# Performance work log

Measured on AMD Instinct MI355X. Metric: run time of the kernel, lower is better.

## Reference

```python
import jax, jax.numpy as jnp
import numpy as np

IN_CH, OUT_CH = 256, 128
HID = 2 * OUT_CH  # 256
N_NODES, N_EDGES = 50000, 800000


def setup_inputs() -> dict:
    key = jax.random.key(0)
    k1, k2, k3, k4, k5, k6, k7 = jax.random.split(key, 7)
    feats = jax.random.normal(k1, (N_NODES, IN_CH), dtype=jnp.float32)
    src = jax.random.randint(k2, (N_EDGES,), 0, N_NODES, dtype=jnp.int64)
    dst = jax.random.randint(k3, (N_EDGES,), 0, N_NODES, dtype=jnp.int64)
    # GraphConv weights: layer0 in->2*out, layer1 2*out->out (Glorot-ish scale)
    W0 = jax.random.normal(k4, (IN_CH, HID), dtype=jnp.float32) / np.sqrt(IN_CH)
    b0 = jnp.zeros((HID,), dtype=jnp.float32)
    W1 = jax.random.normal(k5, (HID, OUT_CH), dtype=jnp.float32) / np.sqrt(HID)
    b1 = jnp.zeros((OUT_CH,), dtype=jnp.float32)
    return {"feats": feats, "src": src, "dst": dst, "W0": W0, "b0": b0, "W1": W1, "b1": b1}


def _graph_conv(x, W, b, src, dst, norm_src, norm_dst, n_nodes):
    # Apply W first (out <= in) to shrink the edge-gather intermediate, as DGL does.
    h = x @ W                                  # [N, out]
    h = h * norm_src[:, None]                  # D_src^-1/2
    msg = h[src]                               # [E, out] irregular gather
    agg = jax.ops.segment_sum(msg, dst, num_segments=n_nodes)  # SpMM
    agg = agg * norm_dst[:, None] + b          # D_dst^-1/2, bias
    return jax.nn.relu(agg)


def reference(feats, src, dst, W0, b0, W1, b1):
    n = feats.shape[0]
    loop = jnp.arange(n, dtype=src.dtype)
    src_sl = jnp.concatenate([src, loop])      # dgl.add_self_loop
    dst_sl = jnpp = jnp.concatenate([dst, loop])
    ones = jnp.ones_like(src_sl, dtype=feats.dtype)
    out_deg = jax.ops.segment_sum(ones, src_sl, num_segments=n)
    in_deg = jax.ops.segment_sum(ones, dst_sl, num_segments=n)
    norm_src = jax.lax.rsqrt(jnp.maximum(out_deg, 1.0))
    norm_dst = jax.lax.rsqrt(jnp.maximum(in_deg, 1.0))
    x = _graph_conv(feats, W0, b0, src_sl, dst_sl, norm_src, norm_dst, n)
    x = _graph_conv(x, W1, b1, src_sl, dst_sl, norm_src, norm_dst, n)
    return x
```

## Files before the change

kernel.cpp:

```cpp
#include <hip/hip_runtime.h>


typedef __attribute__((ext_vector_type(8))) short short8v;
typedef __attribute__((ext_vector_type(4))) float float4v;
typedef __attribute__((ext_vector_type(4))) _Float16 half4v;
typedef __attribute__((ext_vector_type(2))) _Float16 half2v;

__device__ inline unsigned short f2bf(float x) {
  unsigned u = __float_as_uint(x);
  return (unsigned short)((u + 0x7FFFu + ((u >> 16) & 1u)) >> 16);
}
__device__ inline float bf2f(unsigned short b) {
  return __uint_as_float(((unsigned)b) << 16);
}

__global__ __launch_bounds__(256) void k_hist8(const int* __restrict__ src,
                                               const int* __restrict__ dst,
                                               unsigned* __restrict__ cnt,
                                               int N, int E) {
  unsigned xcc;
  asm("s_getreg_b32 %0, hwreg(HW_REG_XCC_ID)" : "=s"(xcc));
  unsigned* my = cnt + (size_t)(xcc & 7) * 2u * (unsigned)N;
  int e = blockIdx.x * 256 + threadIdx.x;
  if (e < E) {
    __hip_atomic_fetch_add(&my[src[e]], 1u, __ATOMIC_RELAXED,
                           __HIP_MEMORY_SCOPE_WORKGROUP);
    __hip_atomic_fetch_add(&my[N + dst[e]], 1u, __ATOMIC_RELAXED,
                           __HIP_MEMORY_SCOPE_WORKGROUP);
  }
}

__global__ __launch_bounds__(256) void k_scan1_norm(
    const unsigned* __restrict__ cnt, int* __restrict__ part,
    int* __restrict__ bsums, float* __restrict__ nsrc,
    float* __restrict__ ndst, int N) {
  __shared__ int s[256];
  int t = threadIdx.x, g = blockIdx.x * 256 + t;
  int od = 0, id = 0;
  if (g < N) {
#pragma unroll
    for (int x = 0; x < 8; ++x) {
      od += cnt[(size_t)x * 2u * (unsigned)N + g];
      id += cnt[(size_t)x * 2u * (unsigned)N + N + g];
    }
    nsrc[g] = rsqrtf((float)(od + 1));
    ndst[g] = rsqrtf((float)(id + 1));
  }
  int v = (g < N) ? id : 0;
  s[t] = v;
  __syncthreads();
  for (int o = 1; o < 256; o <<= 1) {
    int add = (t >= o) ? s[t - o] : 0;
    __syncthreads();
    s[t] += add;
    __syncthreads();
  }
  if (g < N) part[g] = s[t] - v;
  if (t == 255) bsums[blockIdx.x] = s[255];
}

__global__ __launch_bounds__(256) void k_scan2(int* __restrict__ bsums, int nb) {
  __shared__ int s[256];
  int t = threadIdx.x;
  int v = (t < nb) ? bsums[t] : 0;
  s[t] = v;
  __syncthreads();
  for (int o = 1; o < 256; o <<= 1) {
    int add = (t >= o) ? s[t - o] : 0;
    __syncthreads();
    s[t] += add;
    __syncthreads();
  }
  if (t < nb) bsums[t] = s[t] - v;
}

__global__ __launch_bounds__(256) void k_scan3(int* __restrict__ part,
                                               int* __restrict__ cursor,
                                               const int* __restrict__ bsums,
                                               int N, int E) {
  int t = threadIdx.x, g = blockIdx.x * 256 + t;
  if (g < N) {
    int v = part[g] + bsums[blockIdx.x];
    part[g] = v;
    cursor[g] = v;
  }
  if (g == 0) part[N] = E;
}

__global__ __launch_bounds__(256) void k_fill(const int* __restrict__ src,
                                              const int* __restrict__ dst,
                                              int* __restrict__ cursor,
                                              int* __restrict__ colidx, int E) {
  int e = blockIdx.x * 256 + threadIdx.x;
  if (e < E) {
    int s = src[e];
    int p = atomicAdd(&cursor[dst[e]], 1);
    colidx[p] = s;
  }
}

__global__ __launch_bounds__(256) void k_wsplit(const float* __restrict__ W,
                                                short* __restrict__ WtH,
                                                short* __restrict__ WtL,
                                                int NCOL) {
  const int K = 256;
  int idx = blockIdx.x * 256 + threadIdx.x;
  if (idx >= K * NCOL) return;
  int k = idx & (K - 1);
  int n = idx >> 8;
  float v = W[(size_t)k * NCOL + n];
  unsigned short h = f2bf(v);
  unsigned short l = f2bf(v - bf2f(h));
  WtH[(size_t)n * K + k] = (short)h;
  WtL[(size_t)n * K + k] = (short)l;
}

template <int NCOL>
__global__ __launch_bounds__(256) void k_gemm_mfma(
    const float* __restrict__ A, const short* __restrict__ WtH,
    const short* __restrict__ WtL, const float* __restrict__ norm,
    _Float16* __restrict__ out, int M) {
  constexpr int K = 256, BM = 64, BK = 32, PAD = 40, NF = NCOL / 16;
  __shared__ short AH[BM][PAD], AL[BM][PAD];
  __shared__ short BH[NCOL][PAD], BL[NCOL][PAD];
  int tid = threadIdx.x;
  int w = tid >> 6, l = tid & 63;
  int lg = l >> 4, ln = l & 15;
  int row0 = blockIdx.x * BM;

  float4v acc[NF];
#pragma unroll
  for (int i = 0; i < NF; ++i) acc[i] = (float4v){0.f, 0.f, 0.f, 0.f};

  int ar = tid >> 2;
  int akq = (tid & 3) * 8;

  for (int k0 = 0; k0 < K; k0 += BK) {
    float av[8];
    int grow = row0 + ar;
    if (grow < M) {
      const float4* ap =
          reinterpret_cast<const float4*>(&A[(size_t)grow * K + k0 + akq]);
      float4 v0 = ap[0], v1 = ap[1];
      av[0] = v0.x; av[1] = v0.y; av[2] = v0.z; av[3] = v0.w;
      av[4] = v1.x; av[5] = v1.y; av[6] = v1.z; av[7] = v1.w;
    } else {
#pragma unroll
      for (int i = 0; i < 8; ++i) av[i] = 0.f;
    }
    short hh[8], ll[8];
#pragma unroll
    for (int i = 0; i < 8; ++i) {
      unsigned short h = f2bf(av[i]);
      hh[i] = (short)h;
      ll[i] = (short)f2bf(av[i] - bf2f(h));
    }
    *reinterpret_cast<short8v*>(&AH[ar][akq]) = *reinterpret_cast<short8v*>(hh);
    *reinterpret_cast<short8v*>(&AL[ar][akq]) = *reinterpret_cast<short8v*>(ll);

#pragma unroll
    for (int c = 0; c < NCOL / 64; ++c) {
      int chunk = c * 256 + tid;
      int bn = chunk >> 2, q = (chunk & 3) * 8;
      *reinterpret_cast<short8v*>(&BH[bn][q]) =
          *reinterpret_cast<const short8v*>(&WtH[(size_t)bn * K + k0 + q]);
      *reinterpret_cast<short8v*>(&BL[bn][q]) =
          *reinterpret_cast<const short8v*>(&WtL[(size_t)bn * K + k0 + q]);
    }
    __syncthreads();

    short8v aH = *reinterpret_cast<short8v*>(&AH[w * 16 + ln][lg * 8]);
    short8v aL = *reinterpret_cast<short8v*>(&AL[w * 16 + ln][lg * 8]);
#pragma unroll
    for (int nf = 0; nf < NF; ++nf) {
      short8v bHv = *reinterpret_cast<short8v*>(&BH[nf * 16 + ln][lg * 8]);
      short8v bLv = *reinterpret_cast<short8v*>(&BL[nf * 16 + ln][lg * 8]);
      acc[nf] = __builtin_amdgcn_mfma_f32_16x16x32_bf16(aH, bHv, acc[nf], 0, 0, 0);
      acc[nf] = __builtin_amdgcn_mfma_f32_16x16x32_bf16(aH, bLv, acc[nf], 0, 0, 0);
      acc[nf] = __builtin_amdgcn_mfma_f32_16x16x32_bf16(aL, bHv, acc[nf], 0, 0, 0);
    }
    __syncthreads();
  }

  int rbase = row0 + w * 16 + lg * 4;
  float nrm[4];
#pragma unroll
  for (int j = 0; j < 4; ++j)
    nrm[j] = (rbase + j < M) ? norm[rbase + j] : 0.f;
#pragma unroll
  for (int nf = 0; nf < NF; ++nf) {
#pragma unroll
    for (int j = 0; j < 4; ++j) {
      int r = rbase + j;
      if (r < M)
        out[(size_t)r * NCOL + nf * 16 + ln] = (_Float16)(acc[nf][j] * nrm[j]);
    }
  }
}

__global__ __launch_bounds__(256) void k_agg256(
    const _Float16* __restrict__ h, const int* __restrict__ rowptr,
    const int* __restrict__ colidx, const float* __restrict__ nd,
    const float* __restrict__ bias, float* __restrict__ out, int N) {
  int node = blockIdx.x * 4 + (threadIdx.x >> 6);
  int lane = threadIdx.x & 63;
  if (node >= N) return;
  const half4v* hv = reinterpret_cast<const half4v*>(h);
  half4v hs = hv[(size_t)node * 64 + lane];
  float4 acc;
  acc.x = (float)hs[0]; acc.y = (float)hs[1];
  acc.z = (float)hs[2]; acc.w = (float)hs[3];
  int e0 = rowptr[node], e1 = rowptr[node + 1];
  int e = e0;
  for (; e + 7 < e1; e += 8) {
    int si[8];
#pragma unroll
    for (int i = 0; i < 8; ++i) si[i] = colidx[e + i];
    half4v v[8];
#pragma unroll
    for (int i = 0; i < 8; ++i) v[i] = hv[(size_t)si[i] * 64 + lane];
#pragma unroll
    for (int i = 0; i < 8; ++i) {
      acc.x += (float)v[i][0]; acc.y += (float)v[i][1];
      acc.z += (float)v[i][2]; acc.w += (float)v[i][3];
    }
  }
  for (; e < e1; ++e) {
    half4v v0 = hv[(size_t)colidx[e] * 64 + lane];
    acc.x += (float)v0[0]; acc.y += (float)v0[1];
    acc.z += (float)v0[2]; acc.w += (float)v0[3];
  }
  float n = nd[node];
  float4 b = reinterpret_cast<const float4*>(bias)[lane];
  float4 r;
  r.x = fmaxf(fmaf(acc.x, n, b.x), 0.f);
  r.y = fmaxf(fmaf(acc.y, n, b.y), 0.f);
  r.z = fmaxf(fmaf(acc.z, n, b.z), 0.f);
  r.w = fmaxf(fmaf(acc.w, n, b.w), 0.f);
  reinterpret_cast<float4*>(out)[(size_t)node * 64 + lane] = r;
}

__global__ __launch_bounds__(256) void k_agg128(
    const _Float16* __restrict__ h, const int* __restrict__ rowptr,
    const int* __restrict__ colidx, const float* __restrict__ nd,
    const float* __restrict__ bias, float* __restrict__ out, int N) {
  int node = blockIdx.x * 4 + (threadIdx.x >> 6);
  int lane = threadIdx.x & 63;
  if (node >= N) return;
  const half2v* hv = reinterpret_cast<const half2v*>(h);
  half2v hs = hv[(size_t)node * 64 + lane];
  float2 acc;
  acc.x = (float)hs[0]; acc.y = (float)hs[1];
  int e0 = rowptr[node], e1 = rowptr[node + 1];
  int e = e0;
  for (; e + 7 < e1; e += 8) {
    int si[8];
#pragma unroll
    for (int i = 0; i < 8; ++i) si[i] = colidx[e + i];
    half2v v[8];
#pragma unroll
    for (int i = 0; i < 8; ++i) v[i] = hv[(size_t)si[i] * 64 + lane];
#pragma unroll
    for (int i = 0; i < 8; ++i) {
      acc.x += (float)v[i][0]; acc.y += (float)v[i][1];
    }
  }
  for (; e < e1; ++e) {
    half2v v0 = hv[(size_t)colidx[e] * 64 + lane];
    acc.x += (float)v0[0]; acc.y += (float)v0[1];
  }
  float n = nd[node];
  float2 b = reinterpret_cast<const float2*>(bias)[lane];
  float2 r;
  r.x = fmaxf(fmaf(acc.x, n, b.x), 0.f);
  r.y = fmaxf(fmaf(acc.y, n, b.y), 0.f);
  reinterpret_cast<float2*>(out)[(size_t)node * 64 + lane] = r;
}

extern "C" void kernel_launch(void* const* d_in, const int* in_sizes, int n_in,
                              void* d_out, int out_size, void* d_ws, size_t ws_size,
                              hipStream_t stream) {
  const float* feats = (const float*)d_in[0];
  const int* src = (const int*)d_in[1];
  const int* dst = (const int*)d_in[2];
  const float* W0 = (const float*)d_in[3];
  const float* b0 = (const float*)d_in[4];
  const float* W1 = (const float*)d_in[5];
  const float* b1 = (const float*)d_in[6];
  float* out = (float*)d_out;

  const int IN_CH = 256, HID = 256, OUT_CH = 128;
  int N = in_sizes[0] / IN_CH;
  int E = in_sizes[1];

  char* ws = (char*)d_ws;
  size_t off = 0;
  auto alloc = [&](size_t bytes) -> void* {
    void* p = ws + off;
    off += (bytes + 255) & ~(size_t)255;
    return p;
  };
  _Float16* h0 = (_Float16*)alloc((size_t)N * HID * 2);
  float* x1     = (float*)alloc((size_t)N * HID * 4);
  float* nsrc   = (float*)alloc((size_t)N * 4);
  float* ndst   = (float*)alloc((size_t)N * 4);
  unsigned* cnt = (unsigned*)alloc((size_t)8 * 2 * N * 4);
  int*   rowptr = (int*)alloc((size_t)(N + 1) * 4);
  int*   cursor = (int*)alloc((size_t)N * 4);
  int*   colidx = (int*)alloc((size_t)E * 4);
  int*   bsums  = (int*)alloc(1024);
  short* w0h    = (short*)alloc((size_t)HID * IN_CH * 2);
  short* w0l    = (short*)alloc((size_t)HID * IN_CH * 2);
  short* w1h    = (short*)alloc((size_t)OUT_CH * HID * 2);
  short* w1l    = (short*)alloc((size_t)OUT_CH * HID * 2);
  _Float16* h1  = h0;

  hipMemsetAsync(cnt, 0, (size_t)8 * 2 * N * 4, stream);

  int nbE = (E + 255) / 256, nbN = (N + 255) / 256;
  k_hist8<<<nbE, 256, 0, stream>>>(src, dst, cnt, N, E);
  k_scan1_norm<<<nbN, 256, 0, stream>>>(cnt, rowptr, bsums, nsrc, ndst, N);
  k_scan2<<<1, 256, 0, stream>>>(bsums, nbN);
  k_scan3<<<nbN, 256, 0, stream>>>(rowptr, cursor, bsums, N, E);
  k_fill<<<nbE, 256, 0, stream>>>(src, dst, cursor, colidx, E);

  k_wsplit<<<(IN_CH * HID) / 256, 256, 0, stream>>>(W0, w0h, w0l, HID);
  k_wsplit<<<(HID * OUT_CH) / 256, 256, 0, stream>>>(W1, w1h, w1l, OUT_CH);

  int gm = (N + 63) / 64;
  k_gemm_mfma<256><<<gm, 256, 0, stream>>>(feats, w0h, w0l, nsrc, h0, N);
  k_agg256<<<(N + 3) / 4, 256, 0, stream>>>(h0, rowptr, colidx, ndst, b0, x1, N);

  k_gemm_mfma<128><<<gm, 256, 0, stream>>>(x1, w1h, w1l, nsrc, h1, N);
  k_agg128<<<(N + 3) / 4, 256, 0, stream>>>(h1, rowptr, colidx, ndst, b1, out, N);
}
```

Baseline: 398.3 us.

## Slice aggregation by 32-channel column blocks and use per-XCC fill cursors

```diff
diff --git a/kernel.cpp b/kernel.cpp
--- a/kernel.cpp
+++ b/kernel.cpp
@@ -3,7 +3,6 @@
 
 typedef __attribute__((ext_vector_type(8))) short short8v;
 typedef __attribute__((ext_vector_type(4))) float float4v;
-typedef __attribute__((ext_vector_type(4))) _Float16 half4v;
 typedef __attribute__((ext_vector_type(2))) _Float16 half2v;
 
 __device__ inline unsigned short f2bf(float x) {
@@ -75,26 +74,37 @@
 }
 
 __global__ __launch_bounds__(256) void k_scan3(int* __restrict__ part,
-                                               int* __restrict__ cursor,
+                                               int* __restrict__ cursor8,
                                                const int* __restrict__ bsums,
+                                               const unsigned* __restrict__ cnt,
                                                int N, int E) {
   int t = threadIdx.x, g = blockIdx.x * 256 + t;
   if (g < N) {
     int v = part[g] + bsums[blockIdx.x];
     part[g] = v;
-    cursor[g] = v;
+    int run = v;
+#pragma unroll
+    for (int x = 0; x < 8; ++x) {
+      cursor8[(size_t)x * N + g] = run;
+      run += cnt[(size_t)x * 2u * (unsigned)N + N + g];
+    }
   }
   if (g == 0) part[N] = E;
 }
 
-__global__ __launch_bounds__(256) void k_fill(const int* __restrict__ src,
-                                              const int* __restrict__ dst,
-                                              int* __restrict__ cursor,
-                                              int* __restrict__ colidx, int E) {
+__global__ __launch_bounds__(256) void k_fill8(const int* __restrict__ src,
+                                               const int* __restrict__ dst,
+                                               int* __restrict__ cursor8,
+                                               int* __restrict__ colidx,
+                                               int N, int E) {
+  unsigned xcc;
+  asm("s_getreg_b32 %0, hwreg(HW_REG_XCC_ID)" : "=s"(xcc));
+  int* my = cursor8 + (size_t)(xcc & 7) * N;
   int e = blockIdx.x * 256 + threadIdx.x;
   if (e < E) {
     int s = src[e];
-    int p = atomicAdd(&cursor[dst[e]], 1);
+    int p = __hip_atomic_fetch_add(&my[dst[e]], 1, __ATOMIC_RELAXED,
+                                   __HIP_MEMORY_SCOPE_WORKGROUP);
     colidx[p] = s;
   }
 }
@@ -198,83 +208,49 @@
   }
 }
 
-__global__ __launch_bounds__(256) void k_agg256(
+template <int C>
+__global__ __launch_bounds__(256) void k_agg_slice(
     const _Float16* __restrict__ h, const int* __restrict__ rowptr,
     const int* __restrict__ colidx, const float* __restrict__ nd,
     const float* __restrict__ bias, float* __restrict__ out, int N) {
-  int node = blockIdx.x * 4 + (threadIdx.x >> 6);
-  int lane = threadIdx.x & 63;
+  constexpr int NS = C / 32;
+  int slice = blockIdx.x % NS;
+  int node = (blockIdx.x / NS) * 16 + (threadIdx.x >> 4);
+  int l16 = threadIdx.x & 15;
   if (node >= N) return;
-  const half4v* hv = reinterpret_cast<const half4v*>(h);
-  half4v hs = hv[(size_t)node * 64 + lane];
-  float4 acc;
+  int ch0 = slice * 32 + l16 * 2;
+
+  const half2v* hv = reinterpret_cast<const half2v*>(h);
+  half2v hs = hv[((size_t)node * C + ch0) >> 1];
+  float2 acc;
   acc.x = (float)hs[0]; acc.y = (float)hs[1];
-  acc.z = (float)hs[2]; acc.w = (float)hs[3];
+
   int e0 = rowptr[node], e1 = rowptr[node + 1];
   int e = e0;
   for (; e + 7 < e1; e += 8) {
     int si[8];
 #pragma unroll
     for (int i = 0; i < 8; ++i) si[i] = colidx[e + i];
-    half4v v[8];
-#pragma unroll
-    for (int i = 0; i < 8; ++i) v[i] = hv[(size_t)si[i] * 64 + lane];
+    half2v v[8];
+#pragma unroll
+    for (int i = 0; i < 8; ++i) v[i] = hv[((size_t)si[i] * C + ch0) >> 1];
 #pragma unroll
     for (int i = 0; i < 8; ++i) {
-      acc.x += (float)v[i][0]; acc.y += (float)v[i][1];
-      acc.z += (float)v[i][2]; acc.w += (float)v[i][3];
+      acc.x += (float)v[i][0];
+      acc.y += (float)v[i][1];
     }
   }
   for (; e < e1; ++e) {
-    half4v v0 = hv[(size_t)colidx[e] * 64 + lane];
-    acc.x += (float)v0[0]; acc.y += (float)v0[1];
-    acc.z += (float)v0[2]; acc.w += (float)v0[3];
+    half2v v0 = hv[((size_t)colidx[e] * C + ch0) >> 1];
+    acc.x += (float)v0[0];
+    acc.y += (float)v0[1];
   }
   float n = nd[node];
-  float4 b = reinterpret_cast<const float4*>(bias)[lane];
-  float4 r;
-  r.x = fmaxf(fmaf(acc.x, n, b.x), 0.f);
-  r.y = fmaxf(fmaf(acc.y, n, b.y), 0.f);
-  r.z = fmaxf(fmaf(acc.z, n, b.z), 0.f);
-  r.w = fmaxf(fmaf(acc.w, n, b.w), 0.f);
-  reinterpret_cast<float4*>(out)[(size_t)node * 64 + lane] = r;
-}
-
-__global__ __launch_bounds__(256) void k_agg128(
-    const _Float16* __restrict__ h, const int* __restrict__ rowptr,
-    const int* __restrict__ colidx, const float* __restrict__ nd,
-    const float* __restrict__ bias, float* __restrict__ out, int N) {
-  int node = blockIdx.x * 4 + (threadIdx.x >> 6);
-  int lane = threadIdx.x & 63;
-  if (node >= N) return;
-  const half2v* hv = reinterpret_cast<const half2v*>(h);
-  half2v hs = hv[(size_t)node * 64 + lane];
-  float2 acc;
-  acc.x = (float)hs[0]; acc.y = (float)hs[1];
-  int e0 = rowptr[node], e1 = rowptr[node + 1];
-  int e = e0;
-  for (; e + 7 < e1; e += 8) {
-    int si[8];
-#pragma unroll
-    for (int i = 0; i < 8; ++i) si[i] = colidx[e + i];
-    half2v v[8];
-#pragma unroll
-    for (int i = 0; i < 8; ++i) v[i] = hv[(size_t)si[i] * 64 + lane];
-#pragma unroll
-    for (int i = 0; i < 8; ++i) {
-      acc.x += (float)v[i][0]; acc.y += (float)v[i][1];
-    }
-  }
-  for (; e < e1; ++e) {
-    half2v v0 = hv[(size_t)colidx[e] * 64 + lane];
-    acc.x += (float)v0[0]; acc.y += (float)v0[1];
-  }
-  float n = nd[node];
-  float2 b = reinterpret_cast<const float2*>(bias)[lane];
+  float2 b = *reinterpret_cast<const float2*>(&bias[ch0]);
   float2 r;
   r.x = fmaxf(fmaf(acc.x, n, b.x), 0.f);
   r.y = fmaxf(fmaf(acc.y, n, b.y), 0.f);
-  reinterpret_cast<float2*>(out)[(size_t)node * 64 + lane] = r;
+  *reinterpret_cast<float2*>(&out[(size_t)node * C + ch0]) = r;
 }
 
 extern "C" void kernel_launch(void* const* d_in, const int* in_sizes, int n_in,
@@ -306,7 +282,7 @@
   float* ndst   = (float*)alloc((size_t)N * 4);
   unsigned* cnt = (unsigned*)alloc((size_t)8 * 2 * N * 4);
   int*   rowptr = (int*)alloc((size_t)(N + 1) * 4);
-  int*   cursor = (int*)alloc((size_t)N * 4);
+  int*  cursor8 = (int*)alloc((size_t)8 * N * 4);
   int*   colidx = (int*)alloc((size_t)E * 4);
   int*   bsums  = (int*)alloc(1024);
   short* w0h    = (short*)alloc((size_t)HID * IN_CH * 2);
@@ -321,16 +297,17 @@
   k_hist8<<<nbE, 256, 0, stream>>>(src, dst, cnt, N, E);
   k_scan1_norm<<<nbN, 256, 0, stream>>>(cnt, rowptr, bsums, nsrc, ndst, N);
   k_scan2<<<1, 256, 0, stream>>>(bsums, nbN);
-  k_scan3<<<nbN, 256, 0, stream>>>(rowptr, cursor, bsums, N, E);
-  k_fill<<<nbE, 256, 0, stream>>>(src, dst, cursor, colidx, E);
+  k_scan3<<<nbN, 256, 0, stream>>>(rowptr, cursor8, bsums, cnt, N, E);
+  k_fill8<<<nbE, 256, 0, stream>>>(src, dst, cursor8, colidx, N, E);
 
   k_wsplit<<<(IN_CH * HID) / 256, 256, 0, stream>>>(W0, w0h, w0l, HID);
   k_wsplit<<<(HID * OUT_CH) / 256, 256, 0, stream>>>(W1, w1h, w1l, OUT_CH);
 
   int gm = (N + 63) / 64;
+  int ng = (N + 15) / 16;
   k_gemm_mfma<256><<<gm, 256, 0, stream>>>(feats, w0h, w0l, nsrc, h0, N);
-  k_agg256<<<(N + 3) / 4, 256, 0, stream>>>(h0, rowptr, colidx, ndst, b0, x1, N);
+  k_agg_slice<256><<<ng * 8, 256, 0, stream>>>(h0, rowptr, colidx, ndst, b0, x1, N);
 
   k_gemm_mfma<128><<<gm, 256, 0, stream>>>(x1, w1h, w1l, nsrc, h1, N);
-  k_agg128<<<(N + 3) / 4, 256, 0, stream>>>(h1, rowptr, colidx, ndst, b1, out, N);
-}
+  k_agg_slice<128><<<ng * 4, 256, 0, stream>>>(h1, rowptr, colidx, ndst, b1, out, N);
+}
```

New measurement: 446.4 us. 12.1% more time.

## Store hidden activations in fp16 and use per-XCC fill cursors for CSR build

Applied to the files above, without the earlier changes.

```diff
diff --git a/kernel.cpp b/kernel.cpp
--- a/kernel.cpp
+++ b/kernel.cpp
@@ -3,6 +3,7 @@
 
 typedef __attribute__((ext_vector_type(8))) short short8v;
 typedef __attribute__((ext_vector_type(4))) float float4v;
+typedef __attribute__((ext_vector_type(8))) _Float16 half8v;
 typedef __attribute__((ext_vector_type(4))) _Float16 half4v;
 typedef __attribute__((ext_vector_type(2))) _Float16 half2v;
 
@@ -75,26 +76,37 @@
 }
 
 __global__ __launch_bounds__(256) void k_scan3(int* __restrict__ part,
-                                               int* __restrict__ cursor,
+                                               int* __restrict__ cursor8,
                                                const int* __restrict__ bsums,
+                                               const unsigned* __restrict__ cnt,
                                                int N, int E) {
   int t = threadIdx.x, g = blockIdx.x * 256 + t;
   if (g < N) {
     int v = part[g] + bsums[blockIdx.x];
     part[g] = v;
-    cursor[g] = v;
+    int run = v;
+#pragma unroll
+    for (int x = 0; x < 8; ++x) {
+      cursor8[(size_t)x * N + g] = run;
+      run += cnt[(size_t)x * 2u * (unsigned)N + N + g];
+    }
   }
   if (g == 0) part[N] = E;
 }
 
-__global__ __launch_bounds__(256) void k_fill(const int* __restrict__ src,
-                                              const int* __restrict__ dst,
-                                              int* __restrict__ cursor,
-                                              int* __restrict__ colidx, int E) {
+__global__ __launch_bounds__(256) void k_fill8(const int* __restrict__ src,
+                                               const int* __restrict__ dst,
+                                               int* __restrict__ cursor8,
+                                               int* __restrict__ colidx,
+                                               int N, int E) {
+  unsigned xcc;
+  asm("s_getreg_b32 %0, hwreg(HW_REG_XCC_ID)" : "=s"(xcc));
+  int* my = cursor8 + (size_t)(xcc & 7) * N;
   int e = blockIdx.x * 256 + threadIdx.x;
   if (e < E) {
     int s = src[e];
-    int p = atomicAdd(&cursor[dst[e]], 1);
+    int p = __hip_atomic_fetch_add(&my[dst[e]], 1, __ATOMIC_RELAXED,
+                                   __HIP_MEMORY_SCOPE_WORKGROUP);
     colidx[p] = s;
   }
 }
@@ -115,9 +127,9 @@
   WtL[(size_t)n * K + k] = (short)l;
 }
 
-template <int NCOL>
+template <int NCOL, typename AT>
 __global__ __launch_bounds__(256) void k_gemm_mfma(
-    const float* __restrict__ A, const short* __restrict__ WtH,
+    const AT* __restrict__ A, const short* __restrict__ WtH,
     const short* __restrict__ WtL, const float* __restrict__ norm,
     _Float16* __restrict__ out, int M) {
   constexpr int K = 256, BM = 64, BK = 32, PAD = 40, NF = NCOL / 16;
@@ -139,11 +151,18 @@
     float av[8];
     int grow = row0 + ar;
     if (grow < M) {
-      const float4* ap =
-          reinterpret_cast<const float4*>(&A[(size_t)grow * K + k0 + akq]);
-      float4 v0 = ap[0], v1 = ap[1];
-      av[0] = v0.x; av[1] = v0.y; av[2] = v0.z; av[3] = v0.w;
-      av[4] = v1.x; av[5] = v1.y; av[6] = v1.z; av[7] = v1.w;
+      if constexpr (sizeof(AT) == 4) {
+        const float4* ap =
+            reinterpret_cast<const float4*>(&A[(size_t)grow * K + k0 + akq]);
+        float4 v0 = ap[0], v1 = ap[1];
+        av[0] = v0.x; av[1] = v0.y; av[2] = v0.z; av[3] = v0.w;
+        av[4] = v1.x; av[5] = v1.y; av[6] = v1.z; av[7] = v1.w;
+      } else {
+        half8v v =
+            *reinterpret_cast<const half8v*>(&A[(size_t)grow * K + k0 + akq]);
+#pragma unroll
+        for (int i = 0; i < 8; ++i) av[i] = (float)v[i];
+      }
     } else {
 #pragma unroll
       for (int i = 0; i < 8; ++i) av[i] = 0.f;
@@ -198,10 +217,11 @@
   }
 }
 
+template <typename OT>
 __global__ __launch_bounds__(256) void k_agg256(
     const _Float16* __restrict__ h, const int* __restrict__ rowptr,
     const int* __restrict__ colidx, const float* __restrict__ nd,
-    const float* __restrict__ bias, float* __restrict__ out, int N) {
+    const float* __restrict__ bias, OT* __restrict__ out, int N) {
   int node = blockIdx.x * 4 + (threadIdx.x >> 6);
   int lane = threadIdx.x & 63;
   if (node >= N) return;
@@ -232,12 +252,17 @@
   }
   float n = nd[node];
   float4 b = reinterpret_cast<const float4*>(bias)[lane];
-  float4 r;
-  r.x = fmaxf(fmaf(acc.x, n, b.x), 0.f);
-  r.y = fmaxf(fmaf(acc.y, n, b.y), 0.f);
-  r.z = fmaxf(fmaf(acc.z, n, b.z), 0.f);
-  r.w = fmaxf(fmaf(acc.w, n, b.w), 0.f);
-  reinterpret_cast<float4*>(out)[(size_t)node * 64 + lane] = r;
+  float r0 = fmaxf(fmaf(acc.x, n, b.x), 0.f);
+  float r1 = fmaxf(fmaf(acc.y, n, b.y), 0.f);
+  float r2 = fmaxf(fmaf(acc.z, n, b.z), 0.f);
+  float r3 = fmaxf(fmaf(acc.w, n, b.w), 0.f);
+  if constexpr (sizeof(OT) == 2) {
+    half4v r = {(_Float16)r0, (_Float16)r1, (_Float16)r2, (_Float16)r3};
+    reinterpret_cast<half4v*>(out)[(size_t)node * 64 + lane] = r;
+  } else {
+    float4 r = make_float4(r0, r1, r2, r3);
+    reinterpret_cast<float4*>(out)[(size_t)node * 64 + lane] = r;
+  }
 }
 
 __global__ __launch_bounds__(256) void k_agg128(
@@ -301,12 +326,12 @@
     return p;
   };
   _Float16* h0 = (_Float16*)alloc((size_t)N * HID * 2);
-  float* x1     = (float*)alloc((size_t)N * HID * 4);
+  _Float16* x1 = (_Float16*)alloc((size_t)N * HID * 2);
   float* nsrc   = (float*)alloc((size_t)N * 4);
   float* ndst   = (float*)alloc((size_t)N * 4);
   unsigned* cnt = (unsigned*)alloc((size_t)8 * 2 * N * 4);
   int*   rowptr = (int*)alloc((size_t)(N + 1) * 4);
-  int*   cursor = (int*)alloc((size_t)N * 4);
+  int*  cursor8 = (int*)alloc((size_t)8 * N * 4);
   int*   colidx = (int*)alloc((size_t)E * 4);
   int*   bsums  = (int*)alloc(1024);
   short* w0h    = (short*)alloc((size_t)HID * IN_CH * 2);
@@ -321,16 +346,17 @@
   k_hist8<<<nbE, 256, 0, stream>>>(src, dst, cnt, N, E);
   k_scan1_norm<<<nbN, 256, 0, stream>>>(cnt, rowptr, bsums, nsrc, ndst, N);
   k_scan2<<<1, 256, 0, stream>>>(bsums, nbN);
-  k_scan3<<<nbN, 256, 0, stream>>>(rowptr, cursor, bsums, N, E);
-  k_fill<<<nbE, 256, 0, stream>>>(src, dst, cursor, colidx, E);
+  k_scan3<<<nbN, 256, 0, stream>>>(rowptr, cursor8, bsums, cnt, N, E);
+  k_fill8<<<nbE, 256, 0, stream>>>(src, dst, cursor8, colidx, N, E);
 
   k_wsplit<<<(IN_CH * HID) / 256, 256, 0, stream>>>(W0, w0h, w0l, HID);
   k_wsplit<<<(HID * OUT_CH) / 256, 256, 0, stream>>>(W1, w1h, w1l, OUT_CH);
 
   int gm = (N + 63) / 64;
-  k_gemm_mfma<256><<<gm, 256, 0, stream>>>(feats, w0h, w0l, nsrc, h0, N);
-  k_agg256<<<(N + 3) / 4, 256, 0, stream>>>(h0, rowptr, colidx, ndst, b0, x1, N);
-
-  k_gemm_mfma<128><<<gm, 256, 0, stream>>>(x1, w1h, w1l, nsrc, h1, N);
+  k_gemm_mfma<256, float><<<gm, 256, 0, stream>>>(feats, w0h, w0l, nsrc, h0, N);
+  k_agg256<_Float16><<<(N + 3) / 4, 256, 0, stream>>>(h0, rowptr, colidx, ndst,
+                                                      b0, x1, N);
+
+  k_gemm_mfma<128, _Float16><<<gm, 256, 0, stream>>>(x1, w1h, w1l, nsrc, h1, N);
   k_agg128<<<(N + 3) / 4, 256, 0, stream>>>(h1, rowptr, colidx, ndst, b1, out, N);
 }
```

Result: no change. 395.1 us (-0.8%).
